# Kernel optimization log

Hardware: AMD Instinct MI355X
Metric: run time of the kernel (lower is better)

Reference implementation:

```python
import jax, jax.numpy as jnp
import numpy as np

N = 100000
IN_DIM, H1, H2, OUT_DIM = 128, 128, 16, 10
DROP_P = 0.5


def setup_inputs() -> dict:
    key = jax.random.key(0)
    ks = jax.random.split(key, 9)
    x = jax.random.normal(ks[0], (N, IN_DIM), dtype=jnp.float32)
    edge_index = jax.random.randint(ks[1], (2, 1600000), 0, N, dtype=jnp.int64)
    s = lambda k, sh, fan: jax.random.normal(k, sh, jnp.float32) * (1.0 / np.sqrt(fan))
    return {
        "x": x,
        "edge_index": edge_index,
        "W1": s(ks[2], (IN_DIM, H1), IN_DIM),
        "b1": jnp.zeros((H1,), jnp.float32),
        "W2": s(ks[3], (H1, H2), H1),
        "b2": jnp.zeros((H2,), jnp.float32),
        "prelu_a": jnp.array(0.25, jnp.float32),  # nn.PReLU(): single shared parameter
        "Wfc": s(ks[4], (H2, OUT_DIM), H2),
        "bfc": jnp.zeros((OUT_DIM,), jnp.float32),
    }


def _prelu(x, a):
    return jnp.where(x >= 0, x, a * x)


def _dropout(x, key, p=DROP_P):
    keep = jax.random.bernoulli(key, 1.0 - p, x.shape)
    return jnp.where(keep, x / (1.0 - p), 0.0)


def _gcn_norm(edge_index, n):
    # PyG GCNConv default: add self-loops, symmetric deg^-1/2 normalization
    loop = jnp.arange(n, dtype=edge_index.dtype)
    src = jnp.concatenate([edge_index[0], loop])
    dst = jnp.concatenate([edge_index[1], loop])
    deg = jax.ops.segment_sum(jnp.ones_like(src, jnp.float32), dst, num_segments=n)
    dis = jnp.where(deg > 0, jax.lax.rsqrt(deg), 0.0)
    norm = dis[src] * dis[dst]  # [E + N]
    return src, dst, norm


def _gcn_conv(h, src, dst, norm, b, n):
    msg = h[src] * norm[:, None]          # gather + per-edge scale
    agg = jax.ops.segment_sum(msg, dst, num_segments=n)  # scatter-add
    return agg + b


def reference(x, edge_index, W1, b1, W2, b2, prelu_a, Wfc, bfc):
    n = x.shape[0]
    src, dst, norm = _gcn_norm(edge_index, n)
    dk1, dk2 = jax.random.split(jax.random.key(42))
    h = _gcn_conv(x @ W1, src, dst, norm, b1, n)
    h = _dropout(_prelu(h, prelu_a), dk1)
    h = _gcn_conv(h @ W2, src, dst, norm, b2, n)
    h = _dropout(_prelu(h, prelu_a), dk2)
    return h @ Wfc + bfc
```

## Files before the change

kernel.cpp:

```cpp
#include <hip/hip_runtime.h>
#include <stdint.h>

#define G1  128
#define BSH 9
#define BSZ 512

typedef __attribute__((ext_vector_type(8))) _Float16 f16x8;
typedef __attribute__((ext_vector_type(2))) _Float16 f16x2;
typedef __attribute__((ext_vector_type(2))) __fp16 fp16x2r;
typedef __attribute__((ext_vector_type(4))) float f32x4;

#define TF_ROUND(x0, x1, r)                                                    \
  {                                                                            \
    x0 += x1;                                                                  \
    x1 = (x1 << r) | (x1 >> (32 - r));                                         \
    x1 ^= x0;                                                                  \
  }

__host__ __device__ inline void threefry2x32(uint32_t k0, uint32_t k1,
                                             uint32_t x0, uint32_t x1,
                                             uint32_t* o0, uint32_t* o1) {
  uint32_t ks2 = k0 ^ k1 ^ 0x1BD11BDAu;
  x0 += k0; x1 += k1;
  TF_ROUND(x0, x1, 13) TF_ROUND(x0, x1, 15) TF_ROUND(x0, x1, 26) TF_ROUND(x0, x1, 6)
  x0 += k1; x1 += ks2 + 1u;
  TF_ROUND(x0, x1, 17) TF_ROUND(x0, x1, 29) TF_ROUND(x0, x1, 16) TF_ROUND(x0, x1, 24)
  x0 += ks2; x1 += k0 + 2u;
  TF_ROUND(x0, x1, 13) TF_ROUND(x0, x1, 15) TF_ROUND(x0, x1, 26) TF_ROUND(x0, x1, 6)
  x0 += k0; x1 += k1 + 3u;
  TF_ROUND(x0, x1, 17) TF_ROUND(x0, x1, 29) TF_ROUND(x0, x1, 16) TF_ROUND(x0, x1, 24)
  x0 += k1; x1 += ks2 + 4u;
  TF_ROUND(x0, x1, 13) TF_ROUND(x0, x1, 15) TF_ROUND(x0, x1, 26) TF_ROUND(x0, x1, 6)
  x0 += ks2; x1 += k0 + 5u;
  *o0 = x0; *o1 = x1;
}

__device__ inline uint32_t tf_bits32(uint32_t k0, uint32_t k1, uint32_t ctr) {
  uint32_t a, b;
  threefry2x32(k0, k1, 0u, ctr, &a, &b);
  return a ^ b;
}

__device__ inline f16x2 u2h(uint32_t u) {
  union { uint32_t u; f16x2 h; } c; c.u = u; return c.h;
}
__device__ inline uint32_t h2u(f16x2 h) {
  union { uint32_t u; f16x2 h; } c; c.h = h; return c.u;
}
__device__ inline uint32_t pk2h(float a, float b) {
  union { fp16x2r h; uint32_t u; } c;
  c.h = __builtin_amdgcn_cvt_pkrtz(a, b);
  return c.u;
}
__device__ inline uint16_t f2h(float a) {
  union { fp16x2r h; uint32_t u; } c;
  c.h = __builtin_amdgcn_cvt_pkrtz(a, 0.f);
  return (uint16_t)c.u;
}

__global__ __launch_bounds__(256) void k_build1(
    const int* __restrict__ dst, int* __restrict__ hist_t, int E, int NB, int chunk,
    const float* __restrict__ x, const float* __restrict__ W,
    uint16_t* __restrict__ h, int n) {
  __shared__ char smem[(64 * 136 + 128 * 136) * 2];
  const int tid = threadIdx.x;
  if (blockIdx.x < G1) {
    int* hist = (int*)smem;
    for (int b = tid; b < NB; b += 256) hist[b] = 0;
    __syncthreads();
    int e0 = blockIdx.x * chunk;
    int e1 = min(e0 + chunk, E);
    for (int e = e0 + tid; e < e1; e += 256)
      atomicAdd(&hist[dst[e] >> BSH], 1);
    __syncthreads();
    for (int b = tid; b < NB; b += 256)
      hist_t[b * G1 + blockIdx.x] = hist[b];
    return;
  }
  uint16_t (*As)[136] = (uint16_t(*)[136])smem;
  uint16_t (*Bs)[136] = (uint16_t(*)[136])(smem + 64 * 136 * 2);
  const int rowBase = (blockIdx.x - G1) * 64;
  for (int i = tid; i < 64 * 32; i += 256) {
    int r = i >> 5, c4 = i & 31;
    float4 v = make_float4(0.f, 0.f, 0.f, 0.f);
    if (rowBase + r < n)
      v = ((const float4*)(x + (size_t)(rowBase + r) * 128))[c4];
    *(uint2*)&As[r][c4 * 4] = make_uint2(pk2h(v.x, v.y), pk2h(v.z, v.w));
  }
  {
    int k2 = tid >> 7;
    int c = tid & 127;
    for (int kk = 0; kk < 128; kk += 4) {
      int k = kk + k2 * 2;
      *(uint32_t*)&Bs[c][k] = pk2h(W[k * 128 + c], W[(k + 1) * 128 + c]);
    }
  }
  __syncthreads();
  const int wid = tid >> 6;
  const int lane = tid & 63;
  const int l15 = lane & 15;
  const int lhi = lane >> 4;
  f32x4 acc[8];
#pragma unroll
  for (int t = 0; t < 8; ++t) acc[t] = (f32x4){0.f, 0.f, 0.f, 0.f};
  const int arow = wid * 16 + l15;
#pragma unroll
  for (int ks = 0; ks < 4; ++ks) {
    f16x8 a = *(f16x8*)&As[arow][ks * 32 + lhi * 8];
#pragma unroll
    for (int ct = 0; ct < 8; ++ct) {
      f16x8 bfrag = *(f16x8*)&Bs[ct * 16 + l15][ks * 32 + lhi * 8];
      acc[ct] = __builtin_amdgcn_mfma_f32_16x16x32_f16(a, bfrag, acc[ct], 0, 0, 0);
    }
  }
#pragma unroll
  for (int j = 0; j < 4; ++j) {
    int row = rowBase + wid * 16 + lhi * 4 + j;
    if (row < n) {
#pragma unroll
      for (int ct = 0; ct < 8; ++ct)
        h[(size_t)row * 128 + ct * 16 + l15] = f2h(acc[ct][j]);
    }
  }
}

__global__ __launch_bounds__(256) void k_bscatter(
    const int* __restrict__ src, const int* __restrict__ dst,
    const int* __restrict__ hist_t, int* __restrict__ segs,
    uint32_t* __restrict__ ebuf, int E, int NB, int chunk) {
  __shared__ int rowsum[256];
  __shared__ int cur[256];
  const int g = blockIdx.x;
  const int t = threadIdx.x;
  int rs = 0, ps = 0;
  if (t < NB) {
    const int* row = hist_t + t * G1;
    for (int i = 0; i < G1; ++i) {
      int v = row[i];
      rs += v;
      if (i < g) ps += v;
    }
  }
  rowsum[t] = rs;
  __syncthreads();
  for (int off = 1; off < 256; off <<= 1) {
    int tmp = (t >= off) ? rowsum[t - off] : 0;
    __syncthreads();
    rowsum[t] += tmp;
    __syncthreads();
  }
  int rb = rowsum[t] - rs;
  if (t < NB) cur[t] = rb + ps;
  if (g == 0) {
    if (t < NB) segs[t] = rb;
    if (t == 255) segs[NB] = rowsum[255];
  }
  __syncthreads();
  int e0 = g * chunk, e1 = min(e0 + chunk, E);
  for (int e = e0 + t; e < e1; e += 256) {
    int d = dst[e];
    int slot = atomicAdd(&cur[d >> BSH], 1);
    ebuf[slot] = ((uint32_t)src[e] << BSH) | (uint32_t)(d & (BSZ - 1));
  }
}

__global__ __launch_bounds__(256) void k_bfinal(const uint32_t* __restrict__ ebuf,
                                                const int* __restrict__ segs,
                                                int* __restrict__ rowptr,
                                                float* __restrict__ dis,
                                                int* __restrict__ csrc,
                                                int n, int NB, int E) {
  __shared__ int cnt[BSZ];
  __shared__ int sc[256];
  int b = blockIdx.x;
  int t = threadIdx.x;
  int seg0 = segs[b];
  int seg1 = segs[b + 1];
  for (int i = t; i < BSZ; i += 256) cnt[i] = 0;
  __syncthreads();
  for (int i = seg0 + t; i < seg1; i += 256)
    atomicAdd(&cnt[ebuf[i] & (BSZ - 1)], 1);
  __syncthreads();
  int a0 = cnt[2 * t], a1 = cnt[2 * t + 1];
  int s = a0 + a1;
  sc[t] = s;
  __syncthreads();
  for (int off = 1; off < 256; off <<= 1) {
    int tmp = (t >= off) ? sc[t - off] : 0;
    __syncthreads();
    sc[t] += tmp;
    __syncthreads();
  }
  int pre = sc[t] - s;
  int node0 = b * BSZ;
  int p0 = seg0 + pre;
  int p1 = p0 + a0;
  int nd0 = node0 + 2 * t, nd1 = nd0 + 1;
  if (nd0 <= n) rowptr[nd0] = p0;
  if (nd1 <= n) rowptr[nd1] = p1;
  if (nd0 < n) dis[nd0] = rsqrtf((float)(a0 + 1));
  if (nd1 < n) dis[nd1] = rsqrtf((float)(a1 + 1));
  cnt[2 * t] = p0;
  cnt[2 * t + 1] = p1;
  __syncthreads();
  for (int i = seg0 + t; i < seg1; i += 256) {
    uint32_t u = ebuf[i];
    int slot = atomicAdd(&cnt[u & (BSZ - 1)], 1);
    csrc[slot] = (int)(u >> BSH);
  }
  if (b == NB - 1 && t == 0) rowptr[n] = E;
}

__global__ __launch_bounds__(256) void k_gather12(
    const int* __restrict__ rowptr, const int* __restrict__ csrc,
    const float* __restrict__ dis, const uint16_t* __restrict__ h1,
    const float* __restrict__ bias, const float* __restrict__ pa,
    const float* __restrict__ W2, uint32_t* __restrict__ h2,
    int n, uint32_t k0, uint32_t k1) {
  __shared__ uint16_t hs[16][136];
  __shared__ uint16_t Bs[16][136];
  const int tid = threadIdx.x;
  {
    int c = tid & 15;
    int k8 = tid >> 4;
#pragma unroll
    for (int jj = 0; jj < 8; ++jj) {
      int k = k8 * 8 + jj;
      Bs[c][k] = f2h(W2[k * 16 + c]);
    }
  }
  const int wid = tid >> 6;
  const int lane = tid & 63;
  const int q = lane >> 4;
  const int sl = lane & 15;
  const int f0 = 8 * sl + 2 * q;
  const int base = blockIdx.x * 16;
  const uint4* rowbase = (const uint4*)h1;
  const float a = pa[0];
  const float bi0 = bias[f0];
  const float bi1 = bias[f0 + 1];
  for (int i = 0; i < 4; ++i) {
    const int nrow = wid * 4 + i;
    const int v = base + nrow;
    if (v < n) {
      uint32_t jj = (uint32_t)v * 128u + (uint32_t)f0;
      uint32_t bits0 = tf_bits32(k0, k1, jj);
      uint32_t bits1 = tf_bits32(k0, k1, jj + 1);
      float dv = dis[v];
      f16x2 acc0 = u2h(0u), acc1 = u2h(0u), acc2 = u2h(0u), acc3 = u2h(0u);
      if (q == 0) {
        uint4 r = rowbase[(size_t)v * 16 + sl];
        f16x2 w = u2h(pk2h(dv, dv));
        acc0 += u2h(r.x) * w; acc1 += u2h(r.y) * w;
        acc2 += u2h(r.z) * w; acc3 += u2h(r.w) * w;
      }
      int beg = rowptr[v];
      int deg = rowptr[v + 1] - beg;
      for (int bb = 0; bb < deg; bb += 64) {
        int cnt = min(64, deg - bb);
        int idx = bb + lane;
        int sv = v;
        uint32_t wpk = 0u;
        if (idx < deg) {
          sv = csrc[beg + idx];
          float wd = dis[sv];
          wpk = pk2h(wd, wd);
        }
        for (int j = 0; j < cnt; j += 16) {
          int s0 = __shfl(sv, j + q);
          int s1 = __shfl(sv, j + 4 + q);
          int s2 = __shfl(sv, j + 8 + q);
          int s3 = __shfl(sv, j + 12 + q);
          uint32_t w0 = (uint32_t)__shfl((int)wpk, j + q);
          uint32_t w1 = (uint32_t)__shfl((int)wpk, j + 4 + q);
          uint32_t w2 = (uint32_t)__shfl((int)wpk, j + 8 + q);
          uint32_t w3 = (uint32_t)__shfl((int)wpk, j + 12 + q);
          uint4 r0 = rowbase[(size_t)s0 * 16 + sl];
          uint4 r1 = rowbase[(size_t)s1 * 16 + sl];
          uint4 r2 = rowbase[(size_t)s2 * 16 + sl];
          uint4 r3 = rowbase[(size_t)s3 * 16 + sl];
          f16x2 hw0 = u2h(w0), hw1 = u2h(w1), hw2 = u2h(w2), hw3 = u2h(w3);
          acc0 += u2h(r0.x) * hw0; acc1 += u2h(r0.y) * hw0;
          acc2 += u2h(r0.z) * hw0; acc3 += u2h(r0.w) * hw0;
          acc0 += u2h(r1.x) * hw1; acc1 += u2h(r1.y) * hw1;
          acc2 += u2h(r1.z) * hw1; acc3 += u2h(r1.w) * hw1;
          acc0 += u2h(r2.x) * hw2; acc1 += u2h(r2.y) * hw2;
          acc2 += u2h(r2.z) * hw2; acc3 += u2h(r2.w) * hw2;
          acc0 += u2h(r3.x) * hw3; acc1 += u2h(r3.y) * hw3;
          acc2 += u2h(r3.z) * hw3; acc3 += u2h(r3.w) * hw3;
        }
      }
#define COMB(A)                                                                \
  {                                                                            \
    uint32_t u_ = h2u(A);                                                      \
    A = A + u2h((uint32_t)__shfl_xor((int)u_, 16));                            \
    u_ = h2u(A);                                                               \
    A = A + u2h((uint32_t)__shfl_xor((int)u_, 32));                            \
  }
      COMB(acc0) COMB(acc1) COMB(acc2) COMB(acc3)
#undef COMB
      f16x2 p = (q == 0) ? acc0 : (q == 1) ? acc1 : (q == 2) ? acc2 : acc3;
      float v0 = (float)p.x * dv + bi0;
      float v1 = (float)p.y * dv + bi1;
      v0 = v0 >= 0.f ? v0 : a * v0;
      v1 = v1 >= 0.f ? v1 : a * v1;
      float r0 = (bits0 & 0x80000000u) ? 0.f : 2.f * v0;
      float r1 = (bits1 & 0x80000000u) ? 0.f : 2.f * v1;
      *(uint32_t*)&hs[nrow][f0] = pk2h(r0, r1);
    } else {
      *(uint32_t*)&hs[nrow][f0] = 0u;
    }
  }
  __syncthreads();
  if (wid == 0) {
    const int l15 = lane & 15;
    const int lhi = lane >> 4;
    f32x4 acc = (f32x4){0.f, 0.f, 0.f, 0.f};
#pragma unroll
    for (int ks = 0; ks < 4; ++ks) {
      f16x8 af = *(f16x8*)&hs[l15][ks * 32 + lhi * 8];
      f16x8 bf = *(f16x8*)&Bs[l15][ks * 32 + lhi * 8];
      acc = __builtin_amdgcn_mfma_f32_16x16x32_f16(af, bf, acc, 0, 0, 0);
    }
#pragma unroll
    for (int j = 0; j < 4; ++j) {
      int gnode = base + lhi * 4 + j;
      float val = acc[j];
      float pv = __shfl_xor(val, 1);
      if (gnode < n && (l15 & 1) == 0)
        h2[(size_t)gnode * 8 + (l15 >> 1)] = pk2h(val, pv);
    }
  }
}

__global__ __launch_bounds__(256) void k_gather2(
    const int* __restrict__ rowptr, const int* __restrict__ csrc,
    const float* __restrict__ dis, const uint32_t* __restrict__ h2,
    const float* __restrict__ bias, const float* __restrict__ pa,
    const float* __restrict__ Wfc, const float* __restrict__ bfc,
    float* __restrict__ out, int n, uint32_t k0, uint32_t k1) {
  __shared__ float wfc[16][10];
  __shared__ float sbfc[10];
  __shared__ float sval[32][16];
  const int tid = threadIdx.x;
  if (tid < 160) ((float*)wfc)[tid] = Wfc[tid];
  if (tid < 10) sbfc[tid] = bfc[tid];
  __syncthreads();
  int gnode = (blockIdx.x * 256 + tid) >> 3;
  int sub = tid & 7;
  int grp = tid >> 3;
  if (gnode < n) {
    float dv = dis[gnode];
    f16x2 acc = u2h(h2[(size_t)gnode * 8 + sub]) * u2h(pk2h(dv, dv));
    int beg = rowptr[gnode];
    int deg = rowptr[gnode + 1] - beg;
    for (int base = 0; base < deg; base += 8) {
      int cnt = min(8, deg - base);
      int idx = base + sub;
      int sv = gnode;
      uint32_t wpk = 0u;
      if (idx < deg) {
        sv = csrc[beg + idx];
        float wd = dis[sv];
        wpk = pk2h(wd, wd);
      }
      for (int j = 0; j < cnt; j += 4) {
        int s0 = __shfl(sv, j, 8);
        int s1 = __shfl(sv, j + 1, 8);
        int s2 = __shfl(sv, j + 2, 8);
        int s3 = __shfl(sv, j + 3, 8);
        uint32_t w0 = (uint32_t)__shfl((int)wpk, j, 8);
        uint32_t w1 = (uint32_t)__shfl((int)wpk, j + 1, 8);
        uint32_t w2 = (uint32_t)__shfl((int)wpk, j + 2, 8);
        uint32_t w3 = (uint32_t)__shfl((int)wpk, j + 3, 8);
        uint32_t r0 = h2[(size_t)s0 * 8 + sub];
        uint32_t r1 = h2[(size_t)s1 * 8 + sub];
        uint32_t r2 = h2[(size_t)s2 * 8 + sub];
        uint32_t r3 = h2[(size_t)s3 * 8 + sub];
        acc += u2h(r0) * u2h(w0);
        acc += u2h(r1) * u2h(w1);
        acc += u2h(r2) * u2h(w2);
        acc += u2h(r3) * u2h(w3);
      }
    }
    float a = pa[0];
    int kf = sub * 2;
    float v0 = (float)acc.x * dv + bias[kf];
    float v1 = (float)acc.y * dv + bias[kf + 1];
    v0 = v0 >= 0.f ? v0 : a * v0;
    v1 = v1 >= 0.f ? v1 : a * v1;
    uint32_t c0 = (uint32_t)gnode * 16u + (uint32_t)kf;
    uint32_t bits0 = tf_bits32(k0, k1, c0);
    uint32_t bits1 = tf_bits32(k0, k1, c0 + 1);
    sval[grp][kf]     = (bits0 & 0x80000000u) ? 0.f : 2.f * v0;
    sval[grp][kf + 1] = (bits1 & 0x80000000u) ? 0.f : 2.f * v1;
  }
  __syncthreads();
  if (gnode < n && sub < 5) {
    int c = sub * 2;
    float o0 = sbfc[c], o1 = sbfc[c + 1];
#pragma unroll
    for (int k = 0; k < 16; ++k) {
      float hv = sval[grp][k];
      o0 += hv * wfc[k][c];
      o1 += hv * wfc[k][c + 1];
    }
    *(float2*)&out[(size_t)gnode * 10 + c] = make_float2(o0, o1);
  }
}

extern "C" void kernel_launch(void* const* d_in, const int* in_sizes, int n_in,
                              void* d_out, int out_size, void* d_ws, size_t ws_size,
                              hipStream_t stream) {
  const float* x   = (const float*)d_in[0];
  const int*   ei  = (const int*)d_in[1];
  const float* W1  = (const float*)d_in[2];
  const float* b1  = (const float*)d_in[3];
  const float* W2  = (const float*)d_in[4];
  const float* b2  = (const float*)d_in[5];
  const float* pa  = (const float*)d_in[6];
  const float* Wfc = (const float*)d_in[7];
  const float* bfc = (const float*)d_in[8];
  float* out = (float*)d_out;

  const int n = in_sizes[0] / 128;
  const int E = in_sizes[1] / 2;
  const int* src = ei;
  const int* dst = ei + E;

  const int NB = (n + BSZ - 1) / BSZ;
  const int T = NB * G1;
  const int chunk = (E + G1 - 1) / G1;

  char* w = (char*)d_ws;
  auto alloc = [&](size_t bytes) {
    char* p = w;
    w += (bytes + 255) & ~(size_t)255;
    return p;
  };
  float* dis      = (float*)alloc((size_t)n * 4);
  int* rowptr     = (int*)alloc((size_t)(n + 1) * 4);
  int* hist_t     = (int*)alloc((size_t)(T + 1) * 4);
  int* segs       = (int*)alloc((size_t)(NB + 1) * 4);
  uint32_t* ebuf  = (uint32_t*)alloc((size_t)E * 4);
  int* csrc       = (int*)alloc((size_t)E * 4);
  uint16_t* h1f   = (uint16_t*)alloc((size_t)n * 128 * 2);
  uint32_t* h2f   = (uint32_t*)alloc((size_t)n * 8 * 4);

  uint32_t dk1_0, dk1_1, dk2_0, dk2_1;
  threefry2x32(0u, 42u, 0u, 0u, &dk1_0, &dk1_1);
  threefry2x32(0u, 42u, 0u, 1u, &dk2_0, &dk2_1);

  k_build1<<<G1 + (n + 63) / 64, 256, 0, stream>>>(dst, hist_t, E, NB, chunk,
                                                   x, W1, h1f, n);
  k_bscatter<<<G1, 256, 0, stream>>>(src, dst, hist_t, segs, ebuf, E, NB, chunk);
  k_bfinal<<<NB, 256, 0, stream>>>(ebuf, segs, rowptr, dis, csrc, n, NB, E);

  k_gather12<<<(n + 15) / 16, 256, 0, stream>>>(rowptr, csrc, dis, h1f,
                                                b1, pa, W2, h2f, n, dk1_0, dk1_1);

  k_gather2<<<(n * 8 + 255) / 256, 256, 0, stream>>>(rowptr, csrc, dis, h2f,
                                                     b2, pa, Wfc, bfc, out, n,
                                                     dk2_0, dk2_1);
}
```

Measured before the change: 170.9 us.

## Overlap bucket scatter with GEMM1 and vectorize layer-2 gather loads

The GEMM1 work moves out of the histogram kernel and into the bucket-scatter kernel. This lets the scatter pass (global atomics and ebuf writes) run alongside the dense matmul, while the histogram becomes a small standalone kernel. In the layer-2 gather, each 8-lane group now loads full 16-byte rows for 4 neighbors in parallel instead of 4-byte slices, then combines partial fp16 sums with xor shuffles. The gather change cuts per-edge instruction count and widens memory transactions, at the cost of extra shuffle reductions and a changed fp16 summation order.

Result: no change. 169.6 us (-0.8%).

```diff
diff --git a/kernel.cpp b/kernel.cpp
--- a/kernel.cpp
+++ b/kernel.cpp
@@ -58,23 +58,64 @@
   return (uint16_t)c.u;
 }
 
-__global__ __launch_bounds__(256) void k_build1(
-    const int* __restrict__ dst, int* __restrict__ hist_t, int E, int NB, int chunk,
+__global__ __launch_bounds__(256) void k_hist(const int* __restrict__ dst,
+                                              int* __restrict__ hist_t,
+                                              int E, int NB, int chunk) {
+  __shared__ int hist[256];
+  const int tid = threadIdx.x;
+  for (int b = tid; b < NB; b += 256) hist[b] = 0;
+  __syncthreads();
+  int e0 = blockIdx.x * chunk;
+  int e1 = min(e0 + chunk, E);
+  for (int e = e0 + tid; e < e1; e += 256)
+    atomicAdd(&hist[dst[e] >> BSH], 1);
+  __syncthreads();
+  for (int b = tid; b < NB; b += 256)
+    hist_t[b * G1 + blockIdx.x] = hist[b];
+}
+
+__global__ __launch_bounds__(256) void k_bsc_gemm1(
+    const int* __restrict__ src, const int* __restrict__ dst,
+    const int* __restrict__ hist_t, int* __restrict__ segs,
+    uint32_t* __restrict__ ebuf, int E, int NB, int chunk,
     const float* __restrict__ x, const float* __restrict__ W,
     uint16_t* __restrict__ h, int n) {
   __shared__ char smem[(64 * 136 + 128 * 136) * 2];
   const int tid = threadIdx.x;
   if (blockIdx.x < G1) {
-    int* hist = (int*)smem;
-    for (int b = tid; b < NB; b += 256) hist[b] = 0;
+    int* rowsum = (int*)smem;
+    int* cur = ((int*)smem) + 256;
+    const int g = blockIdx.x;
+    int rs = 0, ps = 0;
+    if (tid < NB) {
+      const int* row = hist_t + tid * G1;
+      for (int i = 0; i < G1; ++i) {
+        int v = row[i];
+        rs += v;
+        if (i < g) ps += v;
+      }
+    }
+    rowsum[tid] = rs;
     __syncthreads();
-    int e0 = blockIdx.x * chunk;
-    int e1 = min(e0 + chunk, E);
-    for (int e = e0 + tid; e < e1; e += 256)
-      atomicAdd(&hist[dst[e] >> BSH], 1);
+    for (int off = 1; off < 256; off <<= 1) {
+      int tmp = (tid >= off) ? rowsum[tid - off] : 0;
+      __syncthreads();
+      rowsum[tid] += tmp;
+      __syncthreads();
+    }
+    int rb = rowsum[tid] - rs;
+    if (tid < NB) cur[tid] = rb + ps;
+    if (g == 0) {
+      if (tid < NB) segs[tid] = rb;
+      if (tid == 255) segs[NB] = rowsum[255];
+    }
     __syncthreads();
-    for (int b = tid; b < NB; b += 256)
-      hist_t[b * G1 + blockIdx.x] = hist[b];
+    int e0 = g * chunk, e1 = min(e0 + chunk, E);
+    for (int e = e0 + tid; e < e1; e += 256) {
+      int d = dst[e];
+      int slot = atomicAdd(&cur[d >> BSH], 1);
+      ebuf[slot] = ((uint32_t)src[e] << BSH) | (uint32_t)(d & (BSZ - 1));
+    }
     return;
   }
   uint16_t (*As)[136] = (uint16_t(*)[136])smem;
@@ -121,46 +162,6 @@
       for (int ct = 0; ct < 8; ++ct)
         h[(size_t)row * 128 + ct * 16 + l15] = f2h(acc[ct][j]);
     }
-  }
-}
-
-__global__ __launch_bounds__(256) void k_bscatter(
-    const int* __restrict__ src, const int* __restrict__ dst,
-    const int* __restrict__ hist_t, int* __restrict__ segs,
-    uint32_t* __restrict__ ebuf, int E, int NB, int chunk) {
-  __shared__ int rowsum[256];
-  __shared__ int cur[256];
-  const int g = blockIdx.x;
-  const int t = threadIdx.x;
-  int rs = 0, ps = 0;
-  if (t < NB) {
-    const int* row = hist_t + t * G1;
-    for (int i = 0; i < G1; ++i) {
-      int v = row[i];
-      rs += v;
-      if (i < g) ps += v;
-    }
-  }
-  rowsum[t] = rs;
-  __syncthreads();
-  for (int off = 1; off < 256; off <<= 1) {
-    int tmp = (t >= off) ? rowsum[t - off] : 0;
-    __syncthreads();
-    rowsum[t] += tmp;
-    __syncthreads();
-  }
-  int rb = rowsum[t] - rs;
-  if (t < NB) cur[t] = rb + ps;
-  if (g == 0) {
-    if (t < NB) segs[t] = rb;
-    if (t == 255) segs[NB] = rowsum[255];
-  }
-  __syncthreads();
-  int e0 = g * chunk, e1 = min(e0 + chunk, E);
-  for (int e = e0 + t; e < e1; e += 256) {
-    int d = dst[e];
-    int slot = atomicAdd(&cur[d >> BSH], 1);
-    ebuf[slot] = ((uint32_t)src[e] << BSH) | (uint32_t)(d & (BSZ - 1));
   }
 }
 
@@ -346,17 +347,30 @@
   if (tid < 160) ((float*)wfc)[tid] = Wfc[tid];
   if (tid < 10) sbfc[tid] = bfc[tid];
   __syncthreads();
-  int gnode = (blockIdx.x * 256 + tid) >> 3;
-  int sub = tid & 7;
-  int grp = tid >> 3;
+  const int gnode = (blockIdx.x * 256 + tid) >> 3;
+  const int grp = tid >> 3;
+  const int sub = tid & 7;
+  const int q = sub >> 1;
+  const int sl = sub & 1;
+  const int f0 = 8 * sl + 2 * q;
+  const uint4* rowbase = (const uint4*)h2;
   if (gnode < n) {
+    uint32_t c0 = (uint32_t)gnode * 16u + (uint32_t)f0;
+    uint32_t bits0 = tf_bits32(k0, k1, c0);
+    uint32_t bits1 = tf_bits32(k0, k1, c0 + 1);
     float dv = dis[gnode];
-    f16x2 acc = u2h(h2[(size_t)gnode * 8 + sub]) * u2h(pk2h(dv, dv));
+    f16x2 acc0 = u2h(0u), acc1 = u2h(0u), acc2 = u2h(0u), acc3 = u2h(0u);
+    if (q == 0) {
+      uint4 r = rowbase[(size_t)gnode * 2 + sl];
+      f16x2 w = u2h(pk2h(dv, dv));
+      acc0 += u2h(r.x) * w; acc1 += u2h(r.y) * w;
+      acc2 += u2h(r.z) * w; acc3 += u2h(r.w) * w;
+    }
     int beg = rowptr[gnode];
     int deg = rowptr[gnode + 1] - beg;
-    for (int base = 0; base < deg; base += 8) {
-      int cnt = min(8, deg - base);
-      int idx = base + sub;
+    for (int bb = 0; bb < deg; bb += 8) {
+      int cnt = min(8, deg - bb);
+      int idx = bb + sub;
       int sv = gnode;
       uint32_t wpk = 0u;
       if (idx < deg) {
@@ -365,35 +379,31 @@
         wpk = pk2h(wd, wd);
       }
       for (int j = 0; j < cnt; j += 4) {
-        int s0 = __shfl(sv, j, 8);
-        int s1 = __shfl(sv, j + 1, 8);
-        int s2 = __shfl(sv, j + 2, 8);
-        int s3 = __shfl(sv, j + 3, 8);
-        uint32_t w0 = (uint32_t)__shfl((int)wpk, j, 8);
-        uint32_t w1 = (uint32_t)__shfl((int)wpk, j + 1, 8);
-        uint32_t w2 = (uint32_t)__shfl((int)wpk, j + 2, 8);
-        uint32_t w3 = (uint32_t)__shfl((int)wpk, j + 3, 8);
-        uint32_t r0 = h2[(size_t)s0 * 8 + sub];
-        uint32_t r1 = h2[(size_t)s1 * 8 + sub];
-        uint32_t r2 = h2[(size_t)s2 * 8 + sub];
-        uint32_t r3 = h2[(size_t)s3 * 8 + sub];
-        acc += u2h(r0) * u2h(w0);
-        acc += u2h(r1) * u2h(w1);
-        acc += u2h(r2) * u2h(w2);
-        acc += u2h(r3) * u2h(w3);
+        int s0 = __shfl(sv, j + q, 8);
+        uint32_t w0 = (uint32_t)__shfl((int)wpk, j + q, 8);
+        uint4 r0 = rowbase[(size_t)s0 * 2 + sl];
+        f16x2 hw0 = u2h(w0);
+        acc0 += u2h(r0.x) * hw0; acc1 += u2h(r0.y) * hw0;
+        acc2 += u2h(r0.z) * hw0; acc3 += u2h(r0.w) * hw0;
       }
     }
+#define COMB2(A)                                                               \
+  {                                                                            \
+    uint32_t u_ = h2u(A);                                                      \
+    A = A + u2h((uint32_t)__shfl_xor((int)u_, 2));                             \
+    u_ = h2u(A);                                                               \
+    A = A + u2h((uint32_t)__shfl_xor((int)u_, 4));                             \
+  }
+    COMB2(acc0) COMB2(acc1) COMB2(acc2) COMB2(acc3)
+#undef COMB2
+    f16x2 p = (q == 0) ? acc0 : (q == 1) ? acc1 : (q == 2) ? acc2 : acc3;
     float a = pa[0];
-    int kf = sub * 2;
-    float v0 = (float)acc.x * dv + bias[kf];
-    float v1 = (float)acc.y * dv + bias[kf + 1];
+    float v0 = (float)p.x * dv + bias[f0];
+    float v1 = (float)p.y * dv + bias[f0 + 1];
     v0 = v0 >= 0.f ? v0 : a * v0;
     v1 = v1 >= 0.f ? v1 : a * v1;
-    uint32_t c0 = (uint32_t)gnode * 16u + (uint32_t)kf;
-    uint32_t bits0 = tf_bits32(k0, k1, c0);
-    uint32_t bits1 = tf_bits32(k0, k1, c0 + 1);
-    sval[grp][kf]     = (bits0 & 0x80000000u) ? 0.f : 2.f * v0;
-    sval[grp][kf + 1] = (bits1 & 0x80000000u) ? 0.f : 2.f * v1;
+    sval[grp][f0]     = (bits0 & 0x80000000u) ? 0.f : 2.f * v0;
+    sval[grp][f0 + 1] = (bits1 & 0x80000000u) ? 0.f : 2.f * v1;
   }
   __syncthreads();
   if (gnode < n && sub < 5) {
@@ -451,9 +461,9 @@
   threefry2x32(0u, 42u, 0u, 0u, &dk1_0, &dk1_1);
   threefry2x32(0u, 42u, 0u, 1u, &dk2_0, &dk2_1);
 
-  k_build1<<<G1 + (n + 63) / 64, 256, 0, stream>>>(dst, hist_t, E, NB, chunk,
-                                                   x, W1, h1f, n);
-  k_bscatter<<<G1, 256, 0, stream>>>(src, dst, hist_t, segs, ebuf, E, NB, chunk);
+  k_hist<<<G1, 256, 0, stream>>>(dst, hist_t, E, NB, chunk);
+  k_bsc_gemm1<<<G1 + (n + 63) / 64, 256, 0, stream>>>(
+      src, dst, hist_t, segs, ebuf, E, NB, chunk, x, W1, h1f, n);
   k_bfinal<<<NB, 256, 0, stream>>>(ebuf, segs, rowptr, dis, csrc, n, NB, E);
 
   k_gather12<<<(n + 15) / 16, 256, 0, stream>>>(rowptr, csrc, dis, h1f,
```
